# Kernel optimization log

Measured on AMD Instinct MI355X. Metric: run time of the kernel, lower is better.

## Reference

```python
import jax, jax.numpy as jnp
import numpy as np

N_NODES = 100000
N_EDGES = 1_600_000
F_IN, HID, N_CLS = 128, 64, 32
NEG_SLOPE = 0.2  # PyG GATv2Conv default


def _segment_softmax(scores, seg, num_segments):
    # numerically stable softmax over edges grouped by destination node
    m = jax.ops.segment_max(scores, seg, num_segments=num_segments)
    ex = jnp.exp(scores - m[seg])
    s = jax.ops.segment_sum(ex, seg, num_segments=num_segments)
    return ex / (s[seg] + 1e-16)


def _gatv2_layer(x, src, dst, Wl, bl, Wr, br, att, bias, num_nodes):
    xl = x @ Wl + bl              # source transform  [N, C]
    xr = x @ Wr + br              # target transform  [N, C]
    # per-edge GATv2 attention logit: a . leaky_relu(xl_j + xr_i)
    e = jax.nn.leaky_relu(xl[src] + xr[dst], NEG_SLOPE) @ att  # [E]
    alpha = _segment_softmax(e, dst, num_nodes)                 # [E]
    out = jax.ops.segment_sum(alpha[:, None] * xl[src], dst, num_segments=num_nodes)
    return out + bias


def _add_self_loops(edge_index, n):
    loops = jnp.arange(n, dtype=edge_index.dtype)
    return jnp.concatenate([edge_index, jnp.stack([loops, loops])], axis=1)


def setup_inputs() -> dict:
    key = jax.random.key(0)
    ks = jax.random.split(key, 8)
    s1 = 1.0 / np.sqrt(F_IN)
    s2 = 1.0 / np.sqrt(HID)
    return {
        "x": jax.random.normal(ks[0], (N_NODES, F_IN), jnp.float32),
        "edge_index": jax.random.randint(ks[1], (2, N_EDGES), 0, N_NODES, jnp.int64),
        "W1l": jax.random.normal(ks[2], (F_IN, HID), jnp.float32) * s1,
        "b1l": jnp.zeros((HID,), jnp.float32),
        "W1r": jax.random.normal(ks[3], (F_IN, HID), jnp.float32) * s1,
        "b1r": jnp.zeros((HID,), jnp.float32),
        "att1": jax.random.normal(ks[4], (HID,), jnp.float32) * s2,
        "bias1": jnp.zeros((HID,), jnp.float32),
        "W2l": jax.random.normal(ks[5], (HID, N_CLS), jnp.float32) * s2,
        "b2l": jnp.zeros((N_CLS,), jnp.float32),
        "W2r": jax.random.normal(ks[6], (HID, N_CLS), jnp.float32) * s2,
        "b2r": jnp.zeros((N_CLS,), jnp.float32),
        "att2": jax.random.normal(ks[7], (N_CLS,), jnp.float32) / np.sqrt(N_CLS),
        "bias2": jnp.zeros((N_CLS,), jnp.float32),
    }


def reference(x, edge_index, W1l, b1l, W1r, b1r, att1, bias1,
              W2l, b2l, W2r, b2r, att2, bias2):
    n = x.shape[0]
    ei = _add_self_loops(edge_index, n)
    src, dst = ei[0], ei[1]
    h = jax.nn.relu(_gatv2_layer(x, src, dst, W1l, b1l, W1r, b1r, att1, bias1, n))
    # F.dropout(training=False) is identity in eval mode
    out = _gatv2_layer(h, src, dst, W2l, b2l, W2r, b2r, att2, bias2, n)
    return out
```

## Files before the change

### kernel.cpp

```cpp
#include <hip/hip_runtime.h>
#include <math.h>

#define F_IN 128
#define HID 64
#define NCLS 32
#define NEG 0.2f
#define NBKT 256
#define CHUNK 8192

__device__ __forceinline__ void f4fma(float4& a, float s, const float4& w) {
    a.x = fmaf(s, w.x, a.x);
    a.y = fmaf(s, w.y, a.y);
    a.z = fmaf(s, w.z, a.z);
    a.w = fmaf(s, w.w, a.w);
}


__global__ __launch_bounds__(256) void zeroBuckets(int* __restrict__ bucketSize, int BK) {
    int i = blockIdx.x * 256 + threadIdx.x;
    if (i < BK) bucketSize[i] = 0;
}

__global__ __launch_bounds__(256) void bucketHist(const int* __restrict__ ei,
                                                  int Eorig, int Etot,
                                                  int* __restrict__ bucketSize, int BK) {
    __shared__ int h[512];
    int t = threadIdx.x;
    for (int j = t; j < BK; j += 256) h[j] = 0;
    __syncthreads();
    int base = blockIdx.x * CHUNK;
    int end = base + CHUNK < Etot ? base + CHUNK : Etot;
    for (int i = base + t; i < end; i += 256) {
        int dst = i < Eorig ? ei[Eorig + i] : i - Eorig;
        atomicAdd(&h[dst >> 8], 1);
    }
    __syncthreads();
    for (int j = t; j < BK; j += 256)
        if (h[j]) atomicAdd(&bucketSize[j], h[j]);
}

__global__ __launch_bounds__(256) void bucketScan(const int* __restrict__ bucketSize,
                                                  int* __restrict__ bucketStart,
                                                  int* __restrict__ bucketCursor,
                                                  int BK, int Etot) {
    __shared__ int sd[256];
    int t = threadIdx.x;
    int v0 = (2 * t     < BK) ? bucketSize[2 * t]     : 0;
    int v1 = (2 * t + 1 < BK) ? bucketSize[2 * t + 1] : 0;
    int ts = v0 + v1;
    sd[t] = ts;
    __syncthreads();
    for (int off = 1; off < 256; off <<= 1) {
        int x = (t >= off) ? sd[t - off] : 0;
        __syncthreads();
        sd[t] += x;
        __syncthreads();
    }
    int excl = sd[t] - ts;
    if (2 * t < BK)     { bucketStart[2 * t] = excl;          bucketCursor[2 * t] = excl; }
    if (2 * t + 1 < BK) { bucketStart[2 * t + 1] = excl + v0; bucketCursor[2 * t + 1] = excl + v0; }
    if (t == 255) bucketStart[BK] = Etot;
}

__global__ __launch_bounds__(256) void bucketScatter(const int* __restrict__ ei,
                                                     int Eorig, int Etot,
                                                     int* __restrict__ bucketCursor,
                                                     int2* __restrict__ pairs, int BK) {
    __shared__ int h[512], lbase[512], hcur[512];
    int t = threadIdx.x;
    for (int j = t; j < BK; j += 256) { h[j] = 0; hcur[j] = 0; }
    __syncthreads();
    int base = blockIdx.x * CHUNK;
    int end = base + CHUNK < Etot ? base + CHUNK : Etot;
    for (int i = base + t; i < end; i += 256) {
        int dst = i < Eorig ? ei[Eorig + i] : i - Eorig;
        atomicAdd(&h[dst >> 8], 1);
    }
    __syncthreads();
    for (int j = t; j < BK; j += 256)
        lbase[j] = h[j] ? atomicAdd(&bucketCursor[j], h[j]) : 0;
    __syncthreads();
    for (int i = base + t; i < end; i += 256) {
        int src, dst;
        if (i < Eorig) { src = ei[i]; dst = ei[Eorig + i]; }
        else           { src = dst = i - Eorig; }
        int b = dst >> 8;
        int off = atomicAdd(&hcur[b], 1);
        pairs[lbase[b] + off] = make_int2(src, dst);
    }
}

__global__ __launch_bounds__(256) void bucketCSR(const int2* __restrict__ pairs,
                                                 const int* __restrict__ bucketStart,
                                                 int* __restrict__ rowstart,
                                                 int* __restrict__ cnt,
                                                 int* __restrict__ srclist, int N) {
    __shared__ int c[256], cur[256];
    int t = threadIdx.x;
    int b = blockIdx.x;
    int lo = b * NBKT;
    int eb = bucketStart[b], ee = bucketStart[b + 1];
    c[t] = 0;
    __syncthreads();
    for (int i = eb + t; i < ee; i += 256)
        atomicAdd(&c[pairs[i].y - lo], 1);
    __syncthreads();
    cur[t] = c[t];
    __syncthreads();
    for (int off = 1; off < 256; off <<= 1) {
        int x = (t >= off) ? cur[t - off] : 0;
        __syncthreads();
        cur[t] += x;
        __syncthreads();
    }
    int excl = cur[t] - c[t];
    int node = lo + t;
    if (node < N) { rowstart[node] = eb + excl; cnt[node] = c[t]; }
    __syncthreads();
    cur[t] = excl;
    __syncthreads();
    for (int i = eb + t; i < ee; i += 256) {
        int2 pr = pairs[i];
        int pos = atomicAdd(&cur[pr.y - lo], 1);
        srclist[eb + pos] = pr.x;
    }
}


__global__ __launch_bounds__(256) void transform1(const float* __restrict__ x,
                                                  const float* __restrict__ Wl,
                                                  const float* __restrict__ bl,
                                                  const float* __restrict__ Wr,
                                                  const float* __restrict__ br,
                                                  float* __restrict__ xl,
                                                  float* __restrict__ xr, int N) {
    __shared__ float sW[F_IN * HID];
    __shared__ float sx[64][132];
    const float* W = blockIdx.y ? Wr : Wl;
    const float* b = blockIdx.y ? br : bl;
    float* o       = blockIdx.y ? xr : xl;
    int t = threadIdx.x;
    int nb = blockIdx.x * 64;

#pragma unroll
    for (int j = 0; j < 8; j++) {
        int f = t + j * 256;
        ((float4*)sW)[f] = ((const float4*)W)[f];
    }
    int maxf = (N - nb) * 32;
#pragma unroll
    for (int j = 0; j < 8; j++) {
        int f = t + j * 256;
        int node = f >> 5, kc = f & 31;
        float4 v = {0.f, 0.f, 0.f, 0.f};
        if (f < maxf) v = ((const float4*)(x + (size_t)nb * F_IN))[f];
        *(float4*)&sx[node][kc * 4] = v;
    }
    __syncthreads();

    int c4 = (t & 15) * 4;
    int slot = t >> 4;
    float4 b4 = *(const float4*)(b + c4);
    float4 acc[4] = {b4, b4, b4, b4};

#pragma unroll 4
    for (int k4 = 0; k4 < F_IN / 4; k4++) {
        int k = k4 * 4;
        float4 w0 = *(const float4*)&sW[(k + 0) * HID + c4];
        float4 w1 = *(const float4*)&sW[(k + 1) * HID + c4];
        float4 w2 = *(const float4*)&sW[(k + 2) * HID + c4];
        float4 w3 = *(const float4*)&sW[(k + 3) * HID + c4];
#pragma unroll
        for (int j = 0; j < 4; j++) {
            float4 xv = *(const float4*)&sx[slot + j * 16][k];
            f4fma(acc[j], xv.x, w0);
            f4fma(acc[j], xv.y, w1);
            f4fma(acc[j], xv.z, w2);
            f4fma(acc[j], xv.w, w3);
        }
    }
#pragma unroll
    for (int j = 0; j < 4; j++) {
        int g = nb + slot + j * 16;
        if (g < N) *(float4*)(o + (size_t)g * HID + c4) = acc[j];
    }
}

__global__ __launch_bounds__(256) void transform2(const float* __restrict__ h,
                                                  const float* __restrict__ Wl,
                                                  const float* __restrict__ bl,
                                                  const float* __restrict__ Wr,
                                                  const float* __restrict__ br,
                                                  float* __restrict__ xl,
                                                  float* __restrict__ xr, int N) {
    __shared__ float sWl[HID * NCLS];
    __shared__ float sWr[HID * NCLS];
    __shared__ float sx[128][68];
    int t = threadIdx.x;
    int nb = blockIdx.x * 128;

#pragma unroll
    for (int j = 0; j < 2; j++) {
        int f = t + j * 256;
        ((float4*)sWl)[f] = ((const float4*)Wl)[f];
        ((float4*)sWr)[f] = ((const float4*)Wr)[f];
    }
    int maxf = (N - nb) * 16;
#pragma unroll
    for (int j = 0; j < 8; j++) {
        int f = t + j * 256;
        int node = f >> 4, kc = f & 15;
        float4 v = {0.f, 0.f, 0.f, 0.f};
        if (f < maxf) v = ((const float4*)(h + (size_t)nb * HID))[f];
        v.x = fmaxf(v.x, 0.f);
        v.y = fmaxf(v.y, 0.f);
        v.z = fmaxf(v.z, 0.f);
        v.w = fmaxf(v.w, 0.f);
        *(float4*)&sx[node][kc * 4] = v;
    }
    __syncthreads();

    int c4 = (t & 7) * 4;
    int slot = t >> 3;
    float4 bl4 = *(const float4*)(bl + c4);
    float4 br4 = *(const float4*)(br + c4);
    float4 accl[4] = {bl4, bl4, bl4, bl4};
    float4 accr[4] = {br4, br4, br4, br4};

#pragma unroll 4
    for (int k4 = 0; k4 < HID / 4; k4++) {
        int k = k4 * 4;
        float4 wl0 = *(const float4*)&sWl[(k + 0) * NCLS + c4];
        float4 wl1 = *(const float4*)&sWl[(k + 1) * NCLS + c4];
        float4 wl2 = *(const float4*)&sWl[(k + 2) * NCLS + c4];
        float4 wl3 = *(const float4*)&sWl[(k + 3) * NCLS + c4];
        float4 wr0 = *(const float4*)&sWr[(k + 0) * NCLS + c4];
        float4 wr1 = *(const float4*)&sWr[(k + 1) * NCLS + c4];
        float4 wr2 = *(const float4*)&sWr[(k + 2) * NCLS + c4];
        float4 wr3 = *(const float4*)&sWr[(k + 3) * NCLS + c4];
#pragma unroll
        for (int j = 0; j < 4; j++) {
            float4 xv = *(const float4*)&sx[slot + j * 32][k];
            f4fma(accl[j], xv.x, wl0); f4fma(accr[j], xv.x, wr0);
            f4fma(accl[j], xv.y, wl1); f4fma(accr[j], xv.y, wr1);
            f4fma(accl[j], xv.z, wl2); f4fma(accr[j], xv.z, wr2);
            f4fma(accl[j], xv.w, wl3); f4fma(accr[j], xv.w, wr3);
        }
    }
#pragma unroll
    for (int j = 0; j < 4; j++) {
        int g = nb + slot + j * 32;
        if (g < N) {
            *(float4*)(xl + (size_t)g * NCLS + c4) = accl[j];
            *(float4*)(xr + (size_t)g * NCLS + c4) = accr[j];
        }
    }
}

template <int C>
__global__ __launch_bounds__(256) void fusedAggK(const float* __restrict__ xl,
                                                 const float* __restrict__ xr,
                                                 const float* __restrict__ att,
                                                 const int* __restrict__ rowstart,
                                                 const int* __restrict__ cnt,
                                                 const int* __restrict__ srclist,
                                                 const float* __restrict__ bias,
                                                 float* __restrict__ out, int N) {
    const int LPQ = C / 4;
    const int SLOTS = 64 / LPQ;
    int wid = threadIdx.x >> 6;
    int lane = threadIdx.x & 63;
    int n = blockIdx.x * 4 + wid;
    if (n >= N) return;

    int slot = lane / LPQ;
    int pos = lane % LPQ;
    int c4 = pos * 4;

    float4 xr4 = *(const float4*)(xr + (size_t)n * C + c4);
    float4 at4 = *(const float4*)(att + c4);
    float4 bi4 = *(const float4*)(bias + c4);

    int row = rowstart[n];
    int deg = cnt[n];

    float s = 0.f;
    float4 acc = {0.f, 0.f, 0.f, 0.f};

    for (int cb = 0; cb < deg; cb += 64) {
        int len = deg - cb; if (len > 64) len = 64;
        int li = lane < len ? lane : len - 1;
        int srcreg = srclist[row + cb + li];
        int nbatch = (len + SLOTS - 1) / SLOTS;
#pragma unroll 4
        for (int b = 0; b < nbatch; b++) {
            int eidx = b * SLOTS + slot;
            int src = __shfl(srcreg, eidx, 64);
            float4 v = *(const float4*)(xl + (size_t)src * C + c4);
            float4 u;
            u.x = v.x + xr4.x; u.y = v.y + xr4.y;
            u.z = v.z + xr4.z; u.w = v.w + xr4.w;
            u.x = fmaxf(u.x, NEG * u.x);
            u.y = fmaxf(u.y, NEG * u.y);
            u.z = fmaxf(u.z, NEG * u.z);
            u.w = fmaxf(u.w, NEG * u.w);
            float p = u.x * at4.x;
            p = fmaf(u.y, at4.y, p);
            p = fmaf(u.z, at4.z, p);
            p = fmaf(u.w, at4.w, p);
#pragma unroll
            for (int o = 1; o < LPQ; o <<= 1) p += __shfl_xor(p, o, 64);
            float w = (eidx < len) ? __expf(p) : 0.f;
            s += w;
            acc.x = fmaf(w, v.x, acc.x);
            acc.y = fmaf(w, v.y, acc.y);
            acc.z = fmaf(w, v.z, acc.z);
            acc.w = fmaf(w, v.w, acc.w);
        }
    }
#pragma unroll
    for (int o = LPQ; o < 64; o <<= 1) {
        acc.x += __shfl_xor(acc.x, o, 64);
        acc.y += __shfl_xor(acc.y, o, 64);
        acc.z += __shfl_xor(acc.z, o, 64);
        acc.w += __shfl_xor(acc.w, o, 64);
        s     += __shfl_xor(s,     o, 64);
    }
    if (lane < LPQ) {
        float inv = 1.f / (s + 1e-16f);
        float4 o4;
        o4.x = acc.x * inv + bi4.x;
        o4.y = acc.y * inv + bi4.y;
        o4.z = acc.z * inv + bi4.z;
        o4.w = acc.w * inv + bi4.w;
        *(float4*)(out + (size_t)n * C + c4) = o4;
    }
}

extern "C" void kernel_launch(void* const* d_in, const int* in_sizes, int n_in,
                              void* d_out, int out_size, void* d_ws, size_t ws_size,
                              hipStream_t stream) {
    const float* x     = (const float*)d_in[0];
    const int*   ei    = (const int*)d_in[1];
    const float* W1l   = (const float*)d_in[2];
    const float* b1l   = (const float*)d_in[3];
    const float* W1r   = (const float*)d_in[4];
    const float* b1r   = (const float*)d_in[5];
    const float* att1  = (const float*)d_in[6];
    const float* bias1 = (const float*)d_in[7];
    const float* W2l   = (const float*)d_in[8];
    const float* b2l   = (const float*)d_in[9];
    const float* W2r   = (const float*)d_in[10];
    const float* b2r   = (const float*)d_in[11];
    const float* att2  = (const float*)d_in[12];
    const float* bias2 = (const float*)d_in[13];
    float* out = (float*)d_out;

    int N     = in_sizes[0] / F_IN;
    int Eorig = in_sizes[1] / 2;
    int Etot  = Eorig + N;
    int BK    = (N + NBKT - 1) / NBKT;

    char* p = (char*)d_ws;
    auto alloc = [&](size_t bytes) { void* r = (void*)p; p += (bytes + 255) & ~(size_t)255; return r; };
    float* xl1     = (float*)alloc((size_t)N * HID * 4);
    float* xr1     = (float*)alloc((size_t)N * HID * 4);
    float* h       = (float*)alloc((size_t)N * HID * 4);
    float* xl2     = (float*)alloc((size_t)N * NCLS * 4);
    float* xr2     = (float*)alloc((size_t)N * NCLS * 4);
    int*   cnt     = (int*)alloc((size_t)N * 4);
    int*   rowstart= (int*)alloc((size_t)N * 4);
    int*   srclist = (int*)alloc((size_t)Etot * 4);
    int*   bucketSize   = (int*)alloc(520 * 4);
    int*   bucketStart  = (int*)alloc(520 * 4);
    int*   bucketCursor = (int*)alloc(520 * 4);
    int2*  pairs   = (int2*)xl2;

    int nChunks = (Etot + CHUNK - 1) / CHUNK;

    zeroBuckets<<<2, 256, 0, stream>>>(bucketSize, BK);
    bucketHist<<<nChunks, 256, 0, stream>>>(ei, Eorig, Etot, bucketSize, BK);
    bucketScan<<<1, 256, 0, stream>>>(bucketSize, bucketStart, bucketCursor, BK, Etot);
    bucketScatter<<<nChunks, 256, 0, stream>>>(ei, Eorig, Etot, bucketCursor, pairs, BK);
    bucketCSR<<<BK, 256, 0, stream>>>(pairs, bucketStart, rowstart, cnt, srclist, N);

    transform1<<<dim3((N + 63) / 64, 2), 256, 0, stream>>>(x, W1l, b1l, W1r, b1r,
                                                           xl1, xr1, N);
    fusedAggK<HID><<<(N + 3) / 4, 256, 0, stream>>>(xl1, xr1, att1, rowstart, cnt,
                                                    srclist, bias1, h, N);

    transform2<<<(N + 127) / 128, 256, 0, stream>>>(h, W2l, b2l, W2r, b2r, xl2, xr2, N);
    fusedAggK<NCLS><<<(N + 3) / 4, 256, 0, stream>>>(xl2, xr2, att2, rowstart, cnt,
                                                     srclist, bias2, out, N);
}
```

Before: 357.8 us.

## Store source features in bf16 for gathers and fuse left/right transform

```diff
diff --git a/kernel.cpp b/kernel.cpp
--- a/kernel.cpp
+++ b/kernel.cpp
@@ -13,6 +13,10 @@
     a.y = fmaf(s, w.y, a.y);
     a.z = fmaf(s, w.z, a.z);
     a.w = fmaf(s, w.w, a.w);
+}
+__device__ __forceinline__ unsigned short f2bf(float f) {
+    unsigned u = __float_as_uint(f);
+    return (unsigned short)((u + 0x7FFFu + ((u >> 16) & 1u)) >> 16);
 }
 
 
@@ -126,63 +130,73 @@
     }
 }
 
-
 __global__ __launch_bounds__(256) void transform1(const float* __restrict__ x,
                                                   const float* __restrict__ Wl,
                                                   const float* __restrict__ bl,
                                                   const float* __restrict__ Wr,
                                                   const float* __restrict__ br,
-                                                  float* __restrict__ xl,
+                                                  unsigned short* __restrict__ xlb,
                                                   float* __restrict__ xr, int N) {
-    __shared__ float sW[F_IN * HID];
-    __shared__ float sx[64][132];
-    const float* W = blockIdx.y ? Wr : Wl;
-    const float* b = blockIdx.y ? br : bl;
-    float* o       = blockIdx.y ? xr : xl;
+    __shared__ float sWl[64 * HID];
+    __shared__ float sWr[64 * HID];
+    __shared__ float sx[64][68];
     int t = threadIdx.x;
     int nb = blockIdx.x * 64;
-
-#pragma unroll
-    for (int j = 0; j < 8; j++) {
-        int f = t + j * 256;
-        ((float4*)sW)[f] = ((const float4*)W)[f];
-    }
-    int maxf = (N - nb) * 32;
-#pragma unroll
-    for (int j = 0; j < 8; j++) {
-        int f = t + j * 256;
-        int node = f >> 5, kc = f & 31;
-        float4 v = {0.f, 0.f, 0.f, 0.f};
-        if (f < maxf) v = ((const float4*)(x + (size_t)nb * F_IN))[f];
-        *(float4*)&sx[node][kc * 4] = v;
-    }
-    __syncthreads();
-
     int c4 = (t & 15) * 4;
     int slot = t >> 4;
-    float4 b4 = *(const float4*)(b + c4);
-    float4 acc[4] = {b4, b4, b4, b4};
+    int maxnode = N - nb;
+
+    float4 bl4 = *(const float4*)(bl + c4);
+    float4 br4 = *(const float4*)(br + c4);
+    float4 accl[4] = {bl4, bl4, bl4, bl4};
+    float4 accr[4] = {br4, br4, br4, br4};
+
+    for (int kt = 0; kt < 2; kt++) {
+        if (kt) __syncthreads();
+#pragma unroll
+        for (int j = 0; j < 4; j++) {
+            int f = t + j * 256;
+            ((float4*)sWl)[f] = ((const float4*)Wl)[kt * 1024 + f];
+            ((float4*)sWr)[f] = ((const float4*)Wr)[kt * 1024 + f];
+            int node = f >> 4, kc = f & 15;
+            float4 v = {0.f, 0.f, 0.f, 0.f};
+            if (node < maxnode)
+                v = ((const float4*)x)[(size_t)(nb + node) * 32 + kt * 16 + kc];
+            *(float4*)&sx[node][kc * 4] = v;
+        }
+        __syncthreads();
 
 #pragma unroll 4
-    for (int k4 = 0; k4 < F_IN / 4; k4++) {
-        int k = k4 * 4;
-        float4 w0 = *(const float4*)&sW[(k + 0) * HID + c4];
-        float4 w1 = *(const float4*)&sW[(k + 1) * HID + c4];
-        float4 w2 = *(const float4*)&sW[(k + 2) * HID + c4];
-        float4 w3 = *(const float4*)&sW[(k + 3) * HID + c4];
-#pragma unroll
-        for (int j = 0; j < 4; j++) {
-            float4 xv = *(const float4*)&sx[slot + j * 16][k];
-            f4fma(acc[j], xv.x, w0);
-            f4fma(acc[j], xv.y, w1);
-            f4fma(acc[j], xv.z, w2);
-            f4fma(acc[j], xv.w, w3);
+        for (int k4 = 0; k4 < 16; k4++) {
+            int k = k4 * 4;
+            float4 wl0 = *(const float4*)&sWl[(k + 0) * HID + c4];
+            float4 wl1 = *(const float4*)&sWl[(k + 1) * HID + c4];
+            float4 wl2 = *(const float4*)&sWl[(k + 2) * HID + c4];
+            float4 wl3 = *(const float4*)&sWl[(k + 3) * HID + c4];
+            float4 wr0 = *(const float4*)&sWr[(k + 0) * HID + c4];
+            float4 wr1 = *(const float4*)&sWr[(k + 1) * HID + c4];
+            float4 wr2 = *(const float4*)&sWr[(k + 2) * HID + c4];
+            float4 wr3 = *(const float4*)&sWr[(k + 3) * HID + c4];
+#pragma unroll
+            for (int j = 0; j < 4; j++) {
+                float4 xv = *(const float4*)&sx[slot + j * 16][k];
+                f4fma(accl[j], xv.x, wl0); f4fma(accr[j], xv.x, wr0);
+                f4fma(accl[j], xv.y, wl1); f4fma(accr[j], xv.y, wr1);
+                f4fma(accl[j], xv.z, wl2); f4fma(accr[j], xv.z, wr2);
+                f4fma(accl[j], xv.w, wl3); f4fma(accr[j], xv.w, wr3);
+            }
         }
     }
 #pragma unroll
     for (int j = 0; j < 4; j++) {
         int g = nb + slot + j * 16;
-        if (g < N) *(float4*)(o + (size_t)g * HID + c4) = acc[j];
+        if (g < N) {
+            ushort4 o;
+            o.x = f2bf(accl[j].x); o.y = f2bf(accl[j].y);
+            o.z = f2bf(accl[j].z); o.w = f2bf(accl[j].w);
+            *(ushort4*)(xlb + (size_t)g * HID + c4) = o;
+            *(float4*)(xr + (size_t)g * HID + c4) = accr[j];
+        }
     }
 }
 
@@ -191,7 +205,7 @@
                                                   const float* __restrict__ bl,
                                                   const float* __restrict__ Wr,
                                                   const float* __restrict__ br,
-                                                  float* __restrict__ xl,
+                                                  unsigned short* __restrict__ xlb,
                                                   float* __restrict__ xr, int N) {
     __shared__ float sWl[HID * NCLS];
     __shared__ float sWr[HID * NCLS];
@@ -251,14 +265,17 @@
     for (int j = 0; j < 4; j++) {
         int g = nb + slot + j * 32;
         if (g < N) {
-            *(float4*)(xl + (size_t)g * NCLS + c4) = accl[j];
+            ushort4 o;
+            o.x = f2bf(accl[j].x); o.y = f2bf(accl[j].y);
+            o.z = f2bf(accl[j].z); o.w = f2bf(accl[j].w);
+            *(ushort4*)(xlb + (size_t)g * NCLS + c4) = o;
             *(float4*)(xr + (size_t)g * NCLS + c4) = accr[j];
         }
     }
 }
 
 template <int C>
-__global__ __launch_bounds__(256) void fusedAggK(const float* __restrict__ xl,
+__global__ __launch_bounds__(256) void fusedAggB(const unsigned short* __restrict__ xlb,
                                                  const float* __restrict__ xr,
                                                  const float* __restrict__ att,
                                                  const int* __restrict__ rowstart,
@@ -266,7 +283,7 @@
                                                  const int* __restrict__ srclist,
                                                  const float* __restrict__ bias,
                                                  float* __restrict__ out, int N) {
-    const int LPQ = C / 4;
+    const int LPQ = C / 8;
     const int SLOTS = 64 / LPQ;
     int wid = threadIdx.x >> 6;
     int lane = threadIdx.x & 63;
@@ -275,65 +292,70 @@
 
     int slot = lane / LPQ;
     int pos = lane % LPQ;
-    int c4 = pos * 4;
-
-    float4 xr4 = *(const float4*)(xr + (size_t)n * C + c4);
-    float4 at4 = *(const float4*)(att + c4);
-    float4 bi4 = *(const float4*)(bias + c4);
+    int c8 = pos * 8;
+
+    float xr8[8], at8[8];
+    *(float4*)&xr8[0] = *(const float4*)(xr + (size_t)n * C + c8);
+    *(float4*)&xr8[4] = *(const float4*)(xr + (size_t)n * C + c8 + 4);
+    *(float4*)&at8[0] = *(const float4*)(att + c8);
+    *(float4*)&at8[4] = *(const float4*)(att + c8 + 4);
 
     int row = rowstart[n];
     int deg = cnt[n];
 
     float s = 0.f;
-    float4 acc = {0.f, 0.f, 0.f, 0.f};
+    float acc[8] = {0.f, 0.f, 0.f, 0.f, 0.f, 0.f, 0.f, 0.f};
 
     for (int cb = 0; cb < deg; cb += 64) {
         int len = deg - cb; if (len > 64) len = 64;
         int li = lane < len ? lane : len - 1;
         int srcreg = srclist[row + cb + li];
         int nbatch = (len + SLOTS - 1) / SLOTS;
-#pragma unroll 4
+#pragma unroll 2
         for (int b = 0; b < nbatch; b++) {
             int eidx = b * SLOTS + slot;
             int src = __shfl(srcreg, eidx, 64);
-            float4 v = *(const float4*)(xl + (size_t)src * C + c4);
-            float4 u;
-            u.x = v.x + xr4.x; u.y = v.y + xr4.y;
-            u.z = v.z + xr4.z; u.w = v.w + xr4.w;
-            u.x = fmaxf(u.x, NEG * u.x);
-            u.y = fmaxf(u.y, NEG * u.y);
-            u.z = fmaxf(u.z, NEG * u.z);
-            u.w = fmaxf(u.w, NEG * u.w);
-            float p = u.x * at4.x;
-            p = fmaf(u.y, at4.y, p);
-            p = fmaf(u.z, at4.z, p);
-            p = fmaf(u.w, at4.w, p);
+            uint4 q = *(const uint4*)(xlb + (size_t)src * C + c8);
+            float v[8];
+            v[0] = __uint_as_float(q.x << 16);
+            v[1] = __uint_as_float(q.x & 0xffff0000u);
+            v[2] = __uint_as_float(q.y << 16);
+            v[3] = __uint_as_float(q.y & 0xffff0000u);
+            v[4] = __uint_as_float(q.z << 16);
+            v[5] = __uint_as_float(q.z & 0xffff0000u);
+            v[6] = __uint_as_float(q.w << 16);
+            v[7] = __uint_as_float(q.w & 0xffff0000u);
+            float p = 0.f;
+#pragma unroll
+            for (int c = 0; c < 8; c++) {
+                float u = v[c] + xr8[c];
+                u = fmaxf(u, NEG * u);
+                p = fmaf(u, at8[c], p);
+            }
 #pragma unroll
             for (int o = 1; o < LPQ; o <<= 1) p += __shfl_xor(p, o, 64);
             float w = (eidx < len) ? __expf(p) : 0.f;
             s += w;
-            acc.x = fmaf(w, v.x, acc.x);
-            acc.y = fmaf(w, v.y, acc.y);
-            acc.z = fmaf(w, v.z, acc.z);
-            acc.w = fmaf(w, v.w, acc.w);
+#pragma unroll
+            for (int c = 0; c < 8; c++) acc[c] = fmaf(w, v[c], acc[c]);
         }
     }
 #pragma unroll
     for (int o = LPQ; o < 64; o <<= 1) {
-        acc.x += __shfl_xor(acc.x, o, 64);
-        acc.y += __shfl_xor(acc.y, o, 64);
-        acc.z += __shfl_xor(acc.z, o, 64);
-        acc.w += __shfl_xor(acc.w, o, 64);
-        s     += __shfl_xor(s,     o, 64);
+#pragma unroll
+        for (int c = 0; c < 8; c++) acc[c] += __shfl_xor(acc[c], o, 64);
+        s += __shfl_xor(s, o, 64);
     }
     if (lane < LPQ) {
+        float bi8[8];
+        *(float4*)&bi8[0] = *(const float4*)(bias + c8);
+        *(float4*)&bi8[4] = *(const float4*)(bias + c8 + 4);
         float inv = 1.f / (s + 1e-16f);
-        float4 o4;
-        o4.x = acc.x * inv + bi4.x;
-        o4.y = acc.y * inv + bi4.y;
-        o4.z = acc.z * inv + bi4.z;
-        o4.w = acc.w * inv + bi4.w;
-        *(float4*)(out + (size_t)n * C + c4) = o4;
+        float o8[8];
+#pragma unroll
+        for (int c = 0; c < 8; c++) o8[c] = acc[c] * inv + bi8[c];
+        *(float4*)(out + (size_t)n * C + c8)     = *(float4*)&o8[0];
+        *(float4*)(out + (size_t)n * C + c8 + 4) = *(float4*)&o8[4];
     }
 }
 
@@ -363,10 +385,10 @@
 
     char* p = (char*)d_ws;
     auto alloc = [&](size_t bytes) { void* r = (void*)p; p += (bytes + 255) & ~(size_t)255; return r; };
-    float* xl1     = (float*)alloc((size_t)N * HID * 4);
+    unsigned short* xl1b = (unsigned short*)alloc((size_t)N * HID * 2);
     float* xr1     = (float*)alloc((size_t)N * HID * 4);
     float* h       = (float*)alloc((size_t)N * HID * 4);
-    float* xl2     = (float*)alloc((size_t)N * NCLS * 4);
+    unsigned short* xl2b = (unsigned short*)alloc((size_t)N * NCLS * 2);
     float* xr2     = (float*)alloc((size_t)N * NCLS * 4);
     int*   cnt     = (int*)alloc((size_t)N * 4);
     int*   rowstart= (int*)alloc((size_t)N * 4);
@@ -374,7 +396,7 @@
     int*   bucketSize   = (int*)alloc(520 * 4);
     int*   bucketStart  = (int*)alloc(520 * 4);
     int*   bucketCursor = (int*)alloc(520 * 4);
-    int2*  pairs   = (int2*)xl2;
+    int2*  pairs   = (int2*)xl2b;
 
     int nChunks = (Etot + CHUNK - 1) / CHUNK;
 
@@ -384,12 +406,11 @@
     bucketScatter<<<nChunks, 256, 0, stream>>>(ei, Eorig, Etot, bucketCursor, pairs, BK);
     bucketCSR<<<BK, 256, 0, stream>>>(pairs, bucketStart, rowstart, cnt, srclist, N);
 
-    transform1<<<dim3((N + 63) / 64, 2), 256, 0, stream>>>(x, W1l, b1l, W1r, b1r,
-                                                           xl1, xr1, N);
-    fusedAggK<HID><<<(N + 3) / 4, 256, 0, stream>>>(xl1, xr1, att1, rowstart, cnt,
+    transform1<<<(N + 63) / 64, 256, 0, stream>>>(x, W1l, b1l, W1r, b1r, xl1b, xr1, N);
+    fusedAggB<HID><<<(N + 3) / 4, 256, 0, stream>>>(xl1b, xr1, att1, rowstart, cnt,
                                                     srclist, bias1, h, N);
 
-    transform2<<<(N + 127) / 128, 256, 0, stream>>>(h, W2l, b2l, W2r, b2r, xl2, xr2, N);
-    fusedAggK<NCLS><<<(N + 3) / 4, 256, 0, stream>>>(xl2, xr2, att2, rowstart, cnt,
+    transform2<<<(N + 127) / 128, 256, 0, stream>>>(h, W2l, b2l, W2r, b2r, xl2b, xr2, N);
+    fusedAggB<NCLS><<<(N + 3) / 4, 256, 0, stream>>>(xl2b, xr2, att2, rowstart, cnt,
                                                      srclist, bias2, out, N);
 }
```

Result: no change. 352.0 us (-1.6%).
